# Optimization experiments

Hardware: AMD Instinct MI355X
Metric: run time of the kernel (lower is better)

Reference implementation:

```python
import jax, jax.numpy as jnp
import numpy as np

B, L, V, D, H, DK, NL, M = 4, 1024, 64, 256, 4, 64, 4, 20
FF = 4 * D
EPS = 1e-5


def _rel_table(seq_len, m):
    # abs(i-j), log-bucketed beyond m, clipped to [0, 2m] -> int indices [L, L]
    d = jnp.abs(jnp.arange(seq_len)[:, None] - jnp.arange(seq_len)[None, :]).astype(jnp.float32)
    d = jnp.where(d > m, m + jnp.log2(jnp.maximum(d - m, 1.0)), d)
    return jnp.clip(d, 0, 2 * m).astype(jnp.int32)


def _layer_norm(x, g, b):
    mu = jnp.mean(x, axis=-1, keepdims=True)
    var = jnp.mean(jnp.square(x - mu), axis=-1, keepdims=True)
    return (x - mu) * jax.lax.rsqrt(var + EPS) * g + b


def setup_inputs() -> dict:
    key = jax.random.key(0)
    ks = jax.random.split(key, 16)
    w = lambda i, shape: jax.random.normal(ks[i], shape, jnp.float32) * 0.05
    return {
        "x": jax.random.normal(ks[0], (B, L, V), jnp.float32),
        "emb": w(1, (V, D)),
        "Wq": w(2, (NL, D, H * DK)), "bq": jnp.zeros((NL, H * DK), jnp.float32),
        "Wk": w(3, (NL, D, H * DK)), "bk": jnp.zeros((NL, H * DK), jnp.float32),
        "Wv": w(4, (NL, D, H * DK)), "bv": jnp.zeros((NL, H * DK), jnp.float32),
        "Wo": w(5, (NL, H * DK, D)), "bo": jnp.zeros((NL, D), jnp.float32),
        "rel_k": 1.0 + w(6, (NL, 2 * M + 1, H)),  # multiplicative bias ~1
        "rel_b": w(7, (NL, 2 * M + 1, H)),
        "ln1_g": jnp.ones((NL, D), jnp.float32), "ln1_b": jnp.zeros((NL, D), jnp.float32),
        "W1": w(8, (NL, D, FF)), "b1": jnp.zeros((NL, FF), jnp.float32),
        "W2": w(9, (NL, FF, D)), "b2": jnp.zeros((NL, D), jnp.float32),
        "ln2_g": jnp.ones((NL, D), jnp.float32), "ln2_b": jnp.zeros((NL, D), jnp.float32),
    }


def reference(x, emb, Wq, bq, Wk, bk, Wv, bv, Wo, bo, rel_k, rel_b,
              ln1_g, ln1_b, W1, b1, W2, b2, ln2_g, ln2_b):
    h = x @ emb  # [B, L, D]  (dropout inactive: eval mode)
    table = _rel_table(L, M)  # [L, L] int32
    inv_sqrt_dk = jnp.float32(1.0 / np.sqrt(DK))
    attns = []
    for l in range(NL):
        q = (h @ Wq[l] + bq[l]).reshape(B, L, H, DK)
        k = (h @ Wk[l] + bk[l]).reshape(B, L, H, DK)
        v = (h @ Wv[l] + bv[l]).reshape(B, L, H, DK)
        scores = jnp.einsum('blhk,bmhk->bhlm', q, k) * inv_sqrt_dk
        # per-head relative-position bias (table symmetric, so axis order of L,L is immaterial)
        bias_k = jnp.transpose(rel_k[l][table], (2, 1, 0))  # [H, L, L]
        bias_b = jnp.transpose(rel_b[l][table], (2, 1, 0))  # [H, L, L]
        scores = scores * bias_k[None] + bias_b[None]
        attn = jax.nn.softmax(scores, axis=-1)  # attn dropout inactive (eval)
        attns.append(attn)
        out = jnp.einsum('bhlm,bmhk->blhk', attn, v).reshape(B, L, H * DK) @ Wo[l] + bo[l]
        # FeedForwardNetwork (note: source has NO residual connections)
        y = _layer_norm(out, ln1_g[l], ln1_b[l])
        y = jax.nn.gelu(y @ W1[l] + b1[l], approximate=False) @ W2[l] + b2[l]
        h = _layer_norm(y, ln2_g[l], ln2_b[l])
    avg_attn = jnp.mean(jnp.stack(attns, axis=0), axis=0)  # [B, H, L, L]
    return h.mean(axis=1), avg_attn
```

## Files before the change

### kernel.cpp

```cpp
#include <hip/hip_runtime.h>
#include <hip/hip_bf16.h>
#include <math.h>

#define Bn 4
#define Ln 1024
#define Vn 64
#define Dn 256
#define Hn 4
#define DKn 64
#define NLn 4
#define Mn 20
#define FFn 1024
#define NTOK (Bn * Ln)
#define QKVW 768
#define LOG2E 1.4426950408889634f

typedef __attribute__((ext_vector_type(8))) short bf16x8;
typedef __attribute__((ext_vector_type(4))) float f32x4;

__device__ __forceinline__ ushort f2b(float f) {
    uint u = __float_as_uint(f);
    u += 0x7fff + ((u >> 16) & 1);
    return (ushort)(u >> 16);
}
__device__ __forceinline__ float b2f(ushort u) {
    return __uint_as_float(((uint)u) << 16);
}

__global__ __launch_bounds__(256) void embed_k(const float* __restrict__ X,
                                               const float* __restrict__ E,
                                               ushort* __restrict__ Hb) {
    __shared__ float xs[Vn];
    int n = blockIdx.x, d = threadIdx.x;
    if (threadIdx.x < Vn) xs[threadIdx.x] = X[n * Vn + threadIdx.x];
    __syncthreads();
    float s = 0.f;
#pragma unroll
    for (int v = 0; v < Vn; ++v) s += xs[v] * E[v * Dn + d];
    Hb[(size_t)n * Dn + d] = f2b(s);
}

__global__ __launch_bounds__(256) void relbias_k(const float* __restrict__ rk,
                                                 const float* __restrict__ rb,
                                                 float* __restrict__ bkT,
                                                 float* __restrict__ bbT) {
    int tid = blockIdx.x * 256 + threadIdx.x;
    int dist = tid & 1023;
    int hh = (tid >> 10) & 3;
    int l = tid >> 12;
    float dd = (float)dist;
    if (dist > Mn) dd = (float)Mn + log2f((float)(dist - Mn));
    if (dd > 2.0f * Mn) dd = 2.0f * Mn;
    int idx = (int)dd;
    bkT[tid] = rk[(l * (2 * Mn + 1) + idx) * Hn + hh] * 0.125f * LOG2E;
    bbT[tid] = rb[(l * (2 * Mn + 1) + idx) * Hn + hh] * LOG2E;
}

__global__ __launch_bounds__(256) void prep_bias(const float* __restrict__ bq,
                                                 const float* __restrict__ bk,
                                                 const float* __restrict__ bv,
                                                 float* __restrict__ bqkv) {
    int idx = blockIdx.x * 256 + threadIdx.x;
    int l = idx / QKVW, r = idx - l * QKVW;
    float v;
    if (r < 256)      v = bq[l * 256 + r];
    else if (r < 512) v = bk[l * 256 + r - 256];
    else              v = bv[l * 256 + r - 512];
    bqkv[idx] = v;
}

__global__ __launch_bounds__(256) void transpose_cvt(
    const float* __restrict__ src, ushort* __restrict__ dst,
    int R, int C, int srcLS, int dstLS) {
    __shared__ float s[32][33];
    src += (size_t)blockIdx.z * srcLS;
    dst += (size_t)blockIdx.z * dstLS;
    int r0 = blockIdx.y * 32, c0 = blockIdx.x * 32;
    int tx = threadIdx.x & 31, ty = threadIdx.x >> 5;
#pragma unroll
    for (int ii = 0; ii < 4; ++ii)
        s[ty + 8 * ii][tx] = src[(size_t)(r0 + ty + 8 * ii) * C + c0 + tx];
    __syncthreads();
#pragma unroll
    for (int ii = 0; ii < 4; ++ii)
        dst[(size_t)(c0 + ty + 8 * ii) * R + r0 + tx] = f2b(s[tx][ty + 8 * ii]);
}

__global__ __launch_bounds__(256) void transpose_v(const ushort* __restrict__ qkv,
                                                   ushort* __restrict__ Vt) {
    __shared__ ushort s[32][65];
    int j0 = blockIdx.x * 32;
    int bh = blockIdx.y;
    int b = bh >> 2, hh = bh & 3;
    int t = threadIdx.x;
#pragma unroll
    for (int ii = 0; ii < 8; ++ii) {
        int e = t + 256 * ii;
        int jr = e >> 6, dc = e & 63;
        s[jr][dc] = qkv[(size_t)(b * Ln + j0 + jr) * QKVW + 2 * Dn + hh * DKn + dc];
    }
    __syncthreads();
#pragma unroll
    for (int ii = 0; ii < 8; ++ii) {
        int e = t + 256 * ii;
        int dr = e >> 5, jc = e & 31;
        Vt[(size_t)(bh * DKn + dr) * Ln + j0 + jc] = s[jc][dr];
    }
}

#define GST 40
__global__ __launch_bounds__(256) void gemm_mfma(
    const ushort* __restrict__ A, const ushort* __restrict__ Bt,
    const float* __restrict__ bias, ushort* __restrict__ C,
    int M, int N, int K, int act) {
    __shared__ __align__(16) ushort As[64 * GST];
    __shared__ __align__(16) ushort Bs[64 * GST];
    int t = threadIdx.x;
    int lane = t & 63, w = t >> 6;
    int wm = w >> 1, wn = w & 1;
    int l15 = lane & 15, lg = lane >> 4;
    int mBase = blockIdx.y * 64, nBase = blockIdx.x * 64;
    int lrow = t >> 2, lkc = (t & 3) * 8;
    const ushort* Ap = A + (size_t)(mBase + lrow) * K + lkc;
    const ushort* Bp = Bt + (size_t)(nBase + lrow) * K + lkc;
    f32x4 acc[2][2] = {};
    for (int k0 = 0; k0 < K; k0 += 32) {
        uint4 av = *(const uint4*)(Ap + k0);
        uint4 bv = *(const uint4*)(Bp + k0);
        __syncthreads();
        *(uint4*)&As[lrow * GST + lkc] = av;
        *(uint4*)&Bs[lrow * GST + lkc] = bv;
        __syncthreads();
        bf16x8 a0 = *(const bf16x8*)&As[(wm * 32 + l15) * GST + lg * 8];
        bf16x8 a1 = *(const bf16x8*)&As[(wm * 32 + 16 + l15) * GST + lg * 8];
        bf16x8 b0 = *(const bf16x8*)&Bs[(wn * 32 + l15) * GST + lg * 8];
        bf16x8 b1 = *(const bf16x8*)&Bs[(wn * 32 + 16 + l15) * GST + lg * 8];
        acc[0][0] = __builtin_amdgcn_mfma_f32_16x16x32_bf16(a0, b0, acc[0][0], 0, 0, 0);
        acc[0][1] = __builtin_amdgcn_mfma_f32_16x16x32_bf16(a0, b1, acc[0][1], 0, 0, 0);
        acc[1][0] = __builtin_amdgcn_mfma_f32_16x16x32_bf16(a1, b0, acc[1][0], 0, 0, 0);
        acc[1][1] = __builtin_amdgcn_mfma_f32_16x16x32_bf16(a1, b1, acc[1][1], 0, 0, 0);
    }
#pragma unroll
    for (int ni = 0; ni < 2; ++ni) {
        int col = nBase + wn * 32 + ni * 16 + l15;
        float bc = bias[col];
#pragma unroll
        for (int mi = 0; mi < 2; ++mi) {
            int rb = mBase + wm * 32 + mi * 16 + lg * 4;
#pragma unroll
            for (int j = 0; j < 4; ++j) {
                float v = acc[mi][ni][j] + bc;
                if (act) v = v * 0.5f * (1.0f + erff(v * 0.7071067811865475f));
                C[(size_t)(rb + j) * N + col] = f2b(v);
            }
        }
    }
}

#define PWST 40
__global__ __launch_bounds__(256) void attn_fused(
    const ushort* __restrict__ qkv, const ushort* __restrict__ Vt,
    const float* __restrict__ bkTab, const float* __restrict__ bbTab,
    ushort* __restrict__ ctx, float* __restrict__ avg, int first) {
    __shared__ float bk_l[Ln];
    __shared__ float bb_l[Ln];
    __shared__ __align__(16) ushort Pw[4][2][16 * PWST];
    __shared__ float mm[4][16];
    __shared__ float ll[4][16];
    __shared__ float Opart[4][1024];

    int t = threadIdx.x;
    int lane = t & 63, wn = t >> 6;
    int l15 = lane & 15, lg = lane >> 4;

    int bid = blockIdx.x;
    int xcd = bid & 7, sub = bid >> 3;
    int bh = xcd * 2 + (sub >> 6);
    int q = sub & 63;
    int b = bh >> 2, hh = bh & 3;
    int i0 = q * 16;

#pragma unroll
    for (int ii = 0; ii < 4; ++ii) {
        bk_l[t + 256 * ii] = bkTab[hh * Ln + t + 256 * ii];
        bb_l[t + 256 * ii] = bbTab[hh * Ln + t + 256 * ii];
    }
    __syncthreads();

    bf16x8 qa0, qa1;
    {
        const ushort* qp = qkv + (size_t)(b * Ln + i0 + l15) * QKVW + hh * DKn;
        qa0 = *(const bf16x8*)(qp + lg * 8);
        qa1 = *(const bf16x8*)(qp + 32 + lg * 8);
    }

    const ushort* kbase = qkv + (size_t)(b * Ln) * QKVW + Dn + hh * DKn;

    f32x4 sv[16];
    float m[4] = {-1e30f, -1e30f, -1e30f, -1e30f};
#pragma unroll
    for (int c = 0; c < 16; ++c) {
        const ushort* kp = kbase + (size_t)(c * 64 + wn * 16 + l15) * QKVW;
        bf16x8 k0 = *(const bf16x8*)(kp + lg * 8);
        bf16x8 k1 = *(const bf16x8*)(kp + 32 + lg * 8);
        f32x4 acc = {};
        acc = __builtin_amdgcn_mfma_f32_16x16x32_bf16(qa0, k0, acc, 0, 0, 0);
        acc = __builtin_amdgcn_mfma_f32_16x16x32_bf16(qa1, k1, acc, 0, 0, 0);
        int j = c * 64 + wn * 16 + l15;
#pragma unroll
        for (int r = 0; r < 4; ++r) {
            int i = i0 + lg * 4 + r;
            int dist = (i > j) ? (i - j) : (j - i);
            float s = acc[r] * bk_l[dist] + bb_l[dist];
            sv[c][r] = s;
            m[r] = fmaxf(m[r], s);
        }
    }
#pragma unroll
    for (int mask = 1; mask < 16; mask <<= 1)
#pragma unroll
        for (int r = 0; r < 4; ++r) m[r] = fmaxf(m[r], __shfl_xor(m[r], mask, 64));
    if (l15 == 0)
#pragma unroll
        for (int r = 0; r < 4; ++r) mm[wn][lg * 4 + r] = m[r];
    __syncthreads();
#pragma unroll
    for (int r = 0; r < 4; ++r) {
        int row = lg * 4 + r;
        m[r] = fmaxf(fmaxf(mm[0][row], mm[1][row]), fmaxf(mm[2][row], mm[3][row]));
    }
    float lsum[4] = {0.f, 0.f, 0.f, 0.f};
#pragma unroll
    for (int c = 0; c < 16; ++c)
#pragma unroll
        for (int r = 0; r < 4; ++r) {
            float p = exp2f(sv[c][r] - m[r]);
            sv[c][r] = p;
            lsum[r] += p;
        }
#pragma unroll
    for (int mask = 1; mask < 16; mask <<= 1)
#pragma unroll
        for (int r = 0; r < 4; ++r) lsum[r] += __shfl_xor(lsum[r], mask, 64);
    if (l15 == 0)
#pragma unroll
        for (int r = 0; r < 4; ++r) ll[wn][lg * 4 + r] = lsum[r];
    __syncthreads();
    float invl[4];
#pragma unroll
    for (int r = 0; r < 4; ++r) {
        int row = lg * 4 + r;
        invl[r] = 1.0f / (ll[0][row] + ll[1][row] + ll[2][row] + ll[3][row]);
    }

    const ushort* vbase = Vt + (size_t)bh * DKn * Ln;
    float* avgrow = avg + ((size_t)bh * Ln + i0) * Ln;
    f32x4 acco[4] = {};
#pragma unroll
    for (int p = 0; p < 8; ++p) {
        const int c0 = 2 * p, c1 = 2 * p + 1;
        float aold[2][4];
        if (!first) {
#pragma unroll
            for (int cc = 0; cc < 2; ++cc)
#pragma unroll
                for (int r = 0; r < 4; ++r)
                    aold[cc][r] = avgrow[(size_t)(lg * 4 + r) * Ln +
                                         (c0 + cc) * 64 + wn * 16 + l15];
        }
        float pn[2][4];
#pragma unroll
        for (int cc = 0; cc < 2; ++cc)
#pragma unroll
            for (int r = 0; r < 4; ++r) {
                float pv = sv[c0 + cc][r] * invl[r];
                pn[cc][r] = pv;
                ushort ph = f2b(pv);
                int off = (lg * 4 + r) * PWST + cc * 16 + l15;
                Pw[wn][0][off] = ph;
                Pw[wn][1][off] = f2b(pv - b2f(ph));
            }
        int kcol = (lg < 2 ? c0 : c1) * 64 + wn * 16 + (lg & 1) * 8;
        bf16x8 va0 = *(const bf16x8*)(vbase + (size_t)(0 * 16 + l15) * Ln + kcol);
        bf16x8 va1 = *(const bf16x8*)(vbase + (size_t)(1 * 16 + l15) * Ln + kcol);
        bf16x8 va2 = *(const bf16x8*)(vbase + (size_t)(2 * 16 + l15) * Ln + kcol);
        bf16x8 va3 = *(const bf16x8*)(vbase + (size_t)(3 * 16 + l15) * Ln + kcol);
        bf16x8 pbh = *(const bf16x8*)&Pw[wn][0][l15 * PWST + lg * 8];
        bf16x8 pbl = *(const bf16x8*)&Pw[wn][1][l15 * PWST + lg * 8];
        acco[0] = __builtin_amdgcn_mfma_f32_16x16x32_bf16(va0, pbh, acco[0], 0, 0, 0);
        acco[1] = __builtin_amdgcn_mfma_f32_16x16x32_bf16(va1, pbh, acco[1], 0, 0, 0);
        acco[2] = __builtin_amdgcn_mfma_f32_16x16x32_bf16(va2, pbh, acco[2], 0, 0, 0);
        acco[3] = __builtin_amdgcn_mfma_f32_16x16x32_bf16(va3, pbh, acco[3], 0, 0, 0);
        acco[0] = __builtin_amdgcn_mfma_f32_16x16x32_bf16(va0, pbl, acco[0], 0, 0, 0);
        acco[1] = __builtin_amdgcn_mfma_f32_16x16x32_bf16(va1, pbl, acco[1], 0, 0, 0);
        acco[2] = __builtin_amdgcn_mfma_f32_16x16x32_bf16(va2, pbl, acco[2], 0, 0, 0);
        acco[3] = __builtin_amdgcn_mfma_f32_16x16x32_bf16(va3, pbl, acco[3], 0, 0, 0);
#pragma unroll
        for (int cc = 0; cc < 2; ++cc)
#pragma unroll
            for (int r = 0; r < 4; ++r) {
                float v = 0.25f * pn[cc][r];
                if (!first) v += aold[cc][r];
                avgrow[(size_t)(lg * 4 + r) * Ln + (c0 + cc) * 64 + wn * 16 + l15] = v;
            }
    }

#pragma unroll
    for (int dg = 0; dg < 4; ++dg)
#pragma unroll
        for (int r = 0; r < 4; ++r)
            Opart[wn][(dg * 16 + lg * 4 + r) * 16 + l15] = acco[dg][r];
    __syncthreads();
#pragma unroll
    for (int k = 0; k < 4; ++k) {
        int idx = t + 256 * k;
        float v = Opart[0][idx] + Opart[1][idx] + Opart[2][idx] + Opart[3][idx];
        int dd = idx >> 4, ii = idx & 15;
        ctx[(size_t)(b * Ln + i0 + ii) * Dn + hh * DKn + dd] = f2b(v);
    }
}

__global__ __launch_bounds__(256) void layernorm_k(const ushort* __restrict__ X,
                                                   const float* __restrict__ g,
                                                   const float* __restrict__ bta,
                                                   ushort* __restrict__ Y) {
    int w = threadIdx.x >> 6, lane = threadIdx.x & 63;
    int row = blockIdx.x * 4 + w;
    const ushort* xr = X + (size_t)row * Dn;
    float x[4];
#pragma unroll
    for (int ii = 0; ii < 4; ++ii) x[ii] = b2f(xr[lane + 64 * ii]);
    float s = x[0] + x[1] + x[2] + x[3];
#pragma unroll
    for (int m = 1; m < 64; m <<= 1) s += __shfl_xor(s, m, 64);
    float mu = s * (1.0f / 256.0f);
    float vs = 0.f;
#pragma unroll
    for (int ii = 0; ii < 4; ++ii) {
        float d = x[ii] - mu;
        vs += d * d;
    }
#pragma unroll
    for (int m = 1; m < 64; m <<= 1) vs += __shfl_xor(vs, m, 64);
    float rs = rsqrtf(vs * (1.0f / 256.0f) + 1e-5f);
#pragma unroll
    for (int ii = 0; ii < 4; ++ii) {
        int d = lane + 64 * ii;
        Y[(size_t)row * Dn + d] = f2b((x[ii] - mu) * rs * g[d] + bta[d]);
    }
}

__global__ __launch_bounds__(256) void mean_part_k(const ushort* __restrict__ Hb,
                                                   float* __restrict__ part) {
    int blk = blockIdx.x;
    int b = blk >> 4, g = blk & 15;
    int d = threadIdx.x;
    float s = 0.f;
#pragma unroll
    for (int r = 0; r < 64; ++r)
        s += b2f(Hb[(size_t)(b * Ln + g * 64 + r) * Dn + d]);
    part[(size_t)blk * Dn + d] = s;
}
__global__ __launch_bounds__(256) void mean_final_k(const float* __restrict__ part,
                                                    float* __restrict__ out) {
    int b = blockIdx.x, d = threadIdx.x;
    float s = 0.f;
#pragma unroll
    for (int g = 0; g < 16; ++g) s += part[(size_t)(b * 16 + g) * Dn + d];
    out[b * Dn + d] = s * (1.0f / (float)Ln);
}

extern "C" void kernel_launch(void* const* d_in, const int* in_sizes, int n_in,
                              void* d_out, int out_size, void* d_ws, size_t ws_size,
                              hipStream_t stream) {
    const float* x    = (const float*)d_in[0];
    const float* emb  = (const float*)d_in[1];
    const float* Wq   = (const float*)d_in[2];
    const float* bq   = (const float*)d_in[3];
    const float* Wk   = (const float*)d_in[4];
    const float* bk   = (const float*)d_in[5];
    const float* Wv   = (const float*)d_in[6];
    const float* bv   = (const float*)d_in[7];
    const float* Wo   = (const float*)d_in[8];
    const float* bo   = (const float*)d_in[9];
    const float* rk   = (const float*)d_in[10];
    const float* rb   = (const float*)d_in[11];
    const float* ln1g = (const float*)d_in[12];
    const float* ln1b = (const float*)d_in[13];
    const float* W1   = (const float*)d_in[14];
    const float* b1   = (const float*)d_in[15];
    const float* W2   = (const float*)d_in[16];
    const float* b2   = (const float*)d_in[17];
    const float* ln2g = (const float*)d_in[18];
    const float* ln2b = (const float*)d_in[19];

    float* out = (float*)d_out;
    float* avg = out + Bn * Dn;

    char* ws = (char*)d_ws;
    const size_t MB = 1024 * 1024;
    ushort* hb   = (ushort*)(ws);
    ushort* qkvb = (ushort*)(ws + 2 * MB);
    ushort* ctxb = (ushort*)(ws + 8 * MB);
    ushort* t1   = (ushort*)(ws + 10 * MB);
    ushort* ffb  = (ushort*)(ws + 12 * MB);
    ushort* qkvT = (ushort*)(ws + 20 * MB);
    ushort* WoT  = (ushort*)(ws + 22 * MB);
    ushort* W1T  = (ushort*)(ws + 23 * MB);
    ushort* W2T  = (ushort*)(ws + 25 * MB);
    float*  bqkv = (float*)(ws + 27 * MB);
    float*  bkT  = (float*)(ws + 27 * MB + 65536);
    float*  bbT  = (float*)(ws + 27 * MB + 131072);
    ushort* Vt   = (ushort*)(ws + 30 * MB);
    float*  mpart= (float*)(ws + 33 * MB);

    embed_k<<<NTOK, 256, 0, stream>>>(x, emb, hb);
    relbias_k<<<64, 256, 0, stream>>>(rk, rb, bkT, bbT);
    prep_bias<<<12, 256, 0, stream>>>(bq, bk, bv, bqkv);

    dim3 t88(8, 8, NLn);
    transpose_cvt<<<t88, 256, 0, stream>>>(Wq, qkvT + 0,      256, 256, 65536, 196608);
    transpose_cvt<<<t88, 256, 0, stream>>>(Wk, qkvT + 65536,  256, 256, 65536, 196608);
    transpose_cvt<<<t88, 256, 0, stream>>>(Wv, qkvT + 131072, 256, 256, 65536, 196608);
    transpose_cvt<<<t88, 256, 0, stream>>>(Wo, WoT,           256, 256, 65536, 65536);
    transpose_cvt<<<dim3(32, 8, NLn), 256, 0, stream>>>(W1, W1T, 256, 1024, 262144, 262144);
    transpose_cvt<<<dim3(8, 32, NLn), 256, 0, stream>>>(W2, W2T, 1024, 256, 262144, 262144);

    for (int l = 0; l < NLn; ++l) {
        gemm_mfma<<<dim3(12, 64), 256, 0, stream>>>(
            hb, qkvT + (size_t)l * 196608, bqkv + l * QKVW, qkvb, NTOK, QKVW, Dn, 0);
        transpose_v<<<dim3(32, 16), 256, 0, stream>>>(qkvb, Vt);
        attn_fused<<<1024, 256, 0, stream>>>(
            qkvb, Vt, bkT + l * Hn * Ln, bbT + l * Hn * Ln, ctxb, avg, (l == 0) ? 1 : 0);
        gemm_mfma<<<dim3(4, 64), 256, 0, stream>>>(
            ctxb, WoT + (size_t)l * 65536, bo + l * 256, t1, NTOK, Dn, Dn, 0);
        layernorm_k<<<NTOK / 4, 256, 0, stream>>>(
            t1, ln1g + l * 256, ln1b + l * 256, t1);
        gemm_mfma<<<dim3(16, 64), 256, 0, stream>>>(
            t1, W1T + (size_t)l * 262144, b1 + l * FFn, ffb, NTOK, FFn, Dn, 1);
        gemm_mfma<<<dim3(4, 64), 256, 0, stream>>>(
            ffb, W2T + (size_t)l * 262144, b2 + l * 256, hb, NTOK, Dn, FFn, 0);
        layernorm_k<<<NTOK / 4, 256, 0, stream>>>(
            hb, ln2g + l * 256, ln2b + l * 256, hb);
    }
    mean_part_k<<<64, 256, 0, stream>>>(hb, mpart);
    mean_final_k<<<Bn, 256, 0, stream>>>(mpart, out);
}
```

Before: 410.0 us.

## Store per-layer attention probs as bf16 and average them in a final pass

```diff
diff --git a/kernel.cpp b/kernel.cpp
--- a/kernel.cpp
+++ b/kernel.cpp
@@ -14,6 +14,7 @@
 #define NTOK (Bn * Ln)
 #define QKVW 768
 #define LOG2E 1.4426950408889634f
+#define PELEMS (Bn * Hn * Ln * Ln)
 
 typedef __attribute__((ext_vector_type(8))) short bf16x8;
 typedef __attribute__((ext_vector_type(4))) float f32x4;
@@ -158,10 +159,12 @@
 }
 
 #define PWST 40
+template <int MODE>
 __global__ __launch_bounds__(256) void attn_fused(
     const ushort* __restrict__ qkv, const ushort* __restrict__ Vt,
     const float* __restrict__ bkTab, const float* __restrict__ bbTab,
-    ushort* __restrict__ ctx, float* __restrict__ avg, int first) {
+    ushort* __restrict__ ctx, float* __restrict__ avg,
+    ushort* __restrict__ Pout, int first) {
     __shared__ float bk_l[Ln];
     __shared__ float bb_l[Ln];
     __shared__ __align__(16) ushort Pw[4][2][16 * PWST];
@@ -255,12 +258,14 @@
 
     const ushort* vbase = Vt + (size_t)bh * DKn * Ln;
     float* avgrow = avg + ((size_t)bh * Ln + i0) * Ln;
+    ushort* prow = Pout + ((size_t)bh * Ln + i0) * Ln;
+    int iw = lane >> 2, jq = lane & 3;
     f32x4 acco[4] = {};
 #pragma unroll
     for (int p = 0; p < 8; ++p) {
         const int c0 = 2 * p, c1 = 2 * p + 1;
         float aold[2][4];
-        if (!first) {
+        if (MODE == 0 && !first) {
 #pragma unroll
             for (int cc = 0; cc < 2; ++cc)
 #pragma unroll
@@ -295,14 +300,21 @@
         acco[1] = __builtin_amdgcn_mfma_f32_16x16x32_bf16(va1, pbl, acco[1], 0, 0, 0);
         acco[2] = __builtin_amdgcn_mfma_f32_16x16x32_bf16(va2, pbl, acco[2], 0, 0, 0);
         acco[3] = __builtin_amdgcn_mfma_f32_16x16x32_bf16(va3, pbl, acco[3], 0, 0, 0);
-#pragma unroll
-        for (int cc = 0; cc < 2; ++cc)
-#pragma unroll
-            for (int r = 0; r < 4; ++r) {
-                float v = 0.25f * pn[cc][r];
-                if (!first) v += aold[cc][r];
-                avgrow[(size_t)(lg * 4 + r) * Ln + (c0 + cc) * 64 + wn * 16 + l15] = v;
-            }
+        if (MODE == 0) {
+#pragma unroll
+            for (int cc = 0; cc < 2; ++cc)
+#pragma unroll
+                for (int r = 0; r < 4; ++r) {
+                    float v = 0.25f * pn[cc][r];
+                    if (!first) v += aold[cc][r];
+                    avgrow[(size_t)(lg * 4 + r) * Ln + (c0 + cc) * 64 + wn * 16 + l15] = v;
+                }
+        } else {
+            ushort4 ph0 = *(const ushort4*)&Pw[wn][0][iw * PWST + 0 * 16 + jq * 4];
+            ushort4 ph1 = *(const ushort4*)&Pw[wn][0][iw * PWST + 1 * 16 + jq * 4];
+            *(ushort4*)&prow[(size_t)iw * Ln + c0 * 64 + wn * 16 + jq * 4] = ph0;
+            *(ushort4*)&prow[(size_t)iw * Ln + c1 * 64 + wn * 16 + jq * 4] = ph1;
+        }
     }
 
 #pragma unroll
@@ -318,6 +330,21 @@
         int dd = idx >> 4, ii = idx & 15;
         ctx[(size_t)(b * Ln + i0 + ii) * Dn + hh * DKn + dd] = f2b(v);
     }
+}
+
+__global__ __launch_bounds__(256) void avg_sum_k(const ushort* __restrict__ P,
+                                                 float* __restrict__ avg) {
+    size_t e = ((size_t)blockIdx.x * 256 + threadIdx.x) * 4;
+    ushort4 a = *(const ushort4*)&P[e];
+    ushort4 b4 = *(const ushort4*)&P[(size_t)PELEMS + e];
+    ushort4 c4 = *(const ushort4*)&P[(size_t)2 * PELEMS + e];
+    ushort4 d4 = *(const ushort4*)&P[(size_t)3 * PELEMS + e];
+    float4 o;
+    o.x = 0.25f * (b2f(a.x) + b2f(b4.x) + b2f(c4.x) + b2f(d4.x));
+    o.y = 0.25f * (b2f(a.y) + b2f(b4.y) + b2f(c4.y) + b2f(d4.y));
+    o.z = 0.25f * (b2f(a.z) + b2f(b4.z) + b2f(c4.z) + b2f(d4.z));
+    o.w = 0.25f * (b2f(a.w) + b2f(b4.w) + b2f(c4.w) + b2f(d4.w));
+    *(float4*)&avg[e] = o;
 }
 
 __global__ __launch_bounds__(256) void layernorm_k(const ushort* __restrict__ X,
@@ -413,6 +440,10 @@
     float*  bbT  = (float*)(ws + 27 * MB + 131072);
     ushort* Vt   = (ushort*)(ws + 30 * MB);
     float*  mpart= (float*)(ws + 33 * MB);
+    ushort* Pbuf = (ushort*)(ws + 36 * MB);
+
+    const size_t need = 36 * MB + (size_t)4 * PELEMS * sizeof(ushort);
+    const bool fancy = (ws_size >= need);
 
     embed_k<<<NTOK, 256, 0, stream>>>(x, emb, hb);
     relbias_k<<<64, 256, 0, stream>>>(rk, rb, bkT, bbT);
@@ -430,8 +461,15 @@
         gemm_mfma<<<dim3(12, 64), 256, 0, stream>>>(
             hb, qkvT + (size_t)l * 196608, bqkv + l * QKVW, qkvb, NTOK, QKVW, Dn, 0);
         transpose_v<<<dim3(32, 16), 256, 0, stream>>>(qkvb, Vt);
-        attn_fused<<<1024, 256, 0, stream>>>(
-            qkvb, Vt, bkT + l * Hn * Ln, bbT + l * Hn * Ln, ctxb, avg, (l == 0) ? 1 : 0);
+        if (fancy) {
+            attn_fused<1><<<1024, 256, 0, stream>>>(
+                qkvb, Vt, bkT + l * Hn * Ln, bbT + l * Hn * Ln, ctxb, avg,
+                Pbuf + (size_t)l * PELEMS, (l == 0) ? 1 : 0);
+        } else {
+            attn_fused<0><<<1024, 256, 0, stream>>>(
+                qkvb, Vt, bkT + l * Hn * Ln, bbT + l * Hn * Ln, ctxb, avg,
+                (ushort*)Pbuf, (l == 0) ? 1 : 0);
+        }
         gemm_mfma<<<dim3(4, 64), 256, 0, stream>>>(
             ctxb, WoT + (size_t)l * 65536, bo + l * 256, t1, NTOK, Dn, Dn, 0);
         layernorm_k<<<NTOK / 4, 256, 0, stream>>>(
@@ -443,6 +481,9 @@
         layernorm_k<<<NTOK / 4, 256, 0, stream>>>(
             hb, ln2g + l * 256, ln2b + l * 256, hb);
     }
+    if (fancy) {
+        avg_sum_k<<<PELEMS / (256 * 4), 256, 0, stream>>>(Pbuf, avg);
+    }
     mean_part_k<<<64, 256, 0, stream>>>(hb, mpart);
     mean_final_k<<<Bn, 256, 0, stream>>>(mpart, out);
 }
```

After: 426.4 us. +4.0%, slower.
